# Kernel tuning notes

Measured on AMD Instinct MI355X. Metric: run time of the kernel, lower is better.

## Reference

```python
import jax, jax.numpy as jnp
import numpy as np
import math

B, L, D, K = 1, 2048, 512, 64


def setup_inputs() -> dict:
    key = jax.random.key(0)
    ks = jax.random.split(key, 12)
    w = lambda k, shape: (jax.random.normal(k, shape, jnp.float32) * 0.02)
    return {
        "x": jax.random.normal(ks[0], (B, L, D), jnp.float32),
        # key_encoder: Linear(D,D) -> GELU -> Linear(D,K)  (weights stored (in,out))
        "ke_w1": w(ks[1], (D, D)), "ke_b1": jnp.zeros((D,), jnp.float32),
        "ke_w2": w(ks[2], (D, K)), "ke_b2": jnp.zeros((K,), jnp.float32),
        # query_encoder
        "qe_w1": w(ks[3], (D, D)), "qe_b1": jnp.zeros((D,), jnp.float32),
        "qe_w2": w(ks[4], (D, K)), "qe_b2": jnp.zeros((K,), jnp.float32),
        # to_amp: Linear(D,K) -> Softplus
        "amp_w": w(ks[5], (D, K)), "amp_b": jnp.zeros((K,), jnp.float32),
        # to_value: Linear(D,D)
        "v_w": w(ks[6], (D, D)), "v_b": jnp.zeros((D,), jnp.float32),
        # to_out: LayerNorm(D) -> Linear(D,D)
        "ln_g": jnp.ones((D,), jnp.float32), "ln_b": jnp.zeros((D,), jnp.float32),
        "out_w": w(ks[7], (D, D)), "out_b": jnp.zeros((D,), jnp.float32),
    }


def reference(x, ke_w1, ke_b1, ke_w2, ke_b2, qe_w1, qe_b1, qe_w2, qe_b2,
              amp_w, amp_b, v_w, v_b, ln_g, ln_b, out_w, out_b):
    Bx, Lx, Dx = x.shape
    Kx = amp_w.shape[1]
    gelu = lambda t: jax.nn.gelu(t, approximate=False)  # torch nn.GELU default (exact)

    key_phase = jnp.tanh(gelu(x @ ke_w1 + ke_b1) @ ke_w2 + ke_b2) * math.pi   # (B,L,K)
    query_phase = jnp.tanh(gelu(x @ qe_w1 + qe_b1) @ qe_w2 + qe_b2) * math.pi  # (B,L,K)
    amp = jax.nn.softplus(x @ amp_w + amp_b) + 0.1                             # (B,L,K)
    V = x @ v_w + v_b                                                           # (B,L,D), real

    # complex phasors expressed in real arithmetic (V is real):
    # key_phasor   = amp * exp(i*key_phase)   = kr + i*ki
    # query_phasor = amp * exp(i*query_phase) = qr + i*qi
    kr = amp * jnp.cos(key_phase); ki = amp * jnp.sin(key_phase)
    qr = amp * jnp.cos(query_phase); qi = amp * jnp.sin(query_phase)

    # bound = key_phasor[...,None] * V[...,None,:]; memory = cumsum over L
    mem_r = jnp.cumsum(kr[..., None] * V[..., None, :], axis=1)  # (B,L,K,D)
    mem_i = jnp.cumsum(ki[..., None] * V[..., None, :], axis=1)  # (B,L,K,D)

    # retrieved = Re(memory * conj(query_phasor)).sum(K) = sum_k mem_r*qr + mem_i*qi
    retrieved = (jnp.einsum('blkd,blk->bld', mem_r, qr)
                 + jnp.einsum('blkd,blk->bld', mem_i, qi))        # (B,L,D)

    positions = jnp.arange(1, Lx + 1, dtype=jnp.float32)
    norm = jnp.sqrt(positions * Kx)[None, :, None]
    retrieved = retrieved / norm

    # to_out: LayerNorm(eps=1e-5) then Linear
    mu = retrieved.mean(-1, keepdims=True)
    var = ((retrieved - mu) ** 2).mean(-1, keepdims=True)
    rn = (retrieved - mu) / jnp.sqrt(var + 1e-5) * ln_g + ln_b
    return x + rn @ out_w + out_b
```

## Files before the change

kernel.cpp:

```cpp
#include <hip/hip_runtime.h>
#include <math.h>

#define L_ 2048
#define D_ 512
#define K_ 64

typedef __attribute__((ext_vector_type(8))) short short8;
typedef __attribute__((ext_vector_type(4))) float f32x4;
typedef __attribute__((ext_vector_type(4))) unsigned short us4;

__device__ __forceinline__ unsigned short f2bf(float f) {
    unsigned int u = __builtin_bit_cast(unsigned int, f);
    u += 0x7fffu + ((u >> 16) & 1u);
    return (unsigned short)(u >> 16);
}
__device__ __forceinline__ float bf2f(unsigned int u) {
    return __builtin_bit_cast(float, u << 16);
}
__device__ __forceinline__ f32x4 MFMA(short8 a, short8 b, f32x4 c) {
    return __builtin_amdgcn_mfma_f32_16x16x32_bf16(a, b, c, 0, 0, 0);
}

enum { EPI_BIAS = 0, EPI_GELU = 1, EPI_AMP = 2, EPI_PHASE = 3, EPI_OUT = 4 };

template<int EPI>
__device__ __forceinline__ void gemm_body(
    const unsigned short* __restrict__ A, const unsigned short* __restrict__ Bt,
    const float* __restrict__ bias, int N, int Kd, int m0, int n0,
    unsigned short* __restrict__ Cb, float* __restrict__ Cf,
    const float* __restrict__ extra,
    unsigned short* As, unsigned short* Bs)
{
    const int t = threadIdx.x;
    const int w = t >> 6, lane = t & 63, n_ = lane & 15, quad = lane >> 4;
    const int mh = (w >> 1) * 32, nh = (w & 1) * 32;

    f32x4 acc[2][2];
#pragma unroll
    for (int i = 0; i < 2; i++)
#pragma unroll
        for (int j = 0; j < 2; j++) acc[i][j] = (f32x4){0.f, 0.f, 0.f, 0.f};

    const int sr = t >> 2, sseg = (t & 3) * 16;
    const unsigned short* Ap = &A[(size_t)(m0 + sr) * Kd + sseg];
    const unsigned short* Bp = &Bt[(size_t)(n0 + sr) * Kd + sseg];
    const int swoff = sr * 72 + sseg;

    short8 av0 = *(const short8*)(Ap);
    short8 av1 = *(const short8*)(Ap + 8);
    short8 bv0 = *(const short8*)(Bp);
    short8 bv1 = *(const short8*)(Bp + 8);

    int buf = 0;
    *(short8*)(As + swoff) = av0; *(short8*)(As + swoff + 8) = av1;
    *(short8*)(Bs + swoff) = bv0; *(short8*)(Bs + swoff + 8) = bv1;
    __syncthreads();

    for (int k0 = 0; k0 < Kd; k0 += 64) {
        const bool more = (k0 + 64 < Kd);
        if (more) {
            av0 = *(const short8*)(Ap + k0 + 64);
            av1 = *(const short8*)(Ap + k0 + 72);
            bv0 = *(const short8*)(Bp + k0 + 64);
            bv1 = *(const short8*)(Bp + k0 + 72);
        }
        const unsigned short* Ab = As + buf * 4608;
        const unsigned short* Bb = Bs + buf * 4608;
#pragma unroll
        for (int kc = 0; kc < 2; kc++) {
            short8 a0 = *(const short8*)&Ab[(mh      + n_) * 72 + kc * 32 + quad * 8];
            short8 a1 = *(const short8*)&Ab[(mh + 16 + n_) * 72 + kc * 32 + quad * 8];
            short8 b0 = *(const short8*)&Bb[(nh      + n_) * 72 + kc * 32 + quad * 8];
            short8 b1 = *(const short8*)&Bb[(nh + 16 + n_) * 72 + kc * 32 + quad * 8];
            acc[0][0] = MFMA(a0, b0, acc[0][0]);
            acc[0][1] = MFMA(a0, b1, acc[0][1]);
            acc[1][0] = MFMA(a1, b0, acc[1][0]);
            acc[1][1] = MFMA(a1, b1, acc[1][1]);
        }
        if (more) {
            buf ^= 1;
            unsigned short* Aw = As + buf * 4608 + swoff;
            unsigned short* Bw = Bs + buf * 4608 + swoff;
            *(short8*)Aw = av0; *(short8*)(Aw + 8) = av1;
            *(short8*)Bw = bv0; *(short8*)(Bw + 8) = bv1;
            __syncthreads();
        }
    }

#pragma unroll
    for (int i = 0; i < 2; i++) {
#pragma unroll
        for (int j = 0; j < 2; j++) {
            const int mb = m0 + mh + i * 16 + quad * 4;
            const int nb = n0 + nh + j * 16 + n_;
            const float bsv = bias[nb];
#pragma unroll
            for (int reg = 0; reg < 4; reg++) {
                const int m = mb + reg;
                float v = acc[i][j][reg] + bsv;
                if (EPI == EPI_GELU) {
                    v = 0.5f * v * (1.0f + erff(v * 0.70710678118654752f));
                    Cb[(size_t)m * N + nb] = f2bf(v);
                } else if (EPI == EPI_BIAS) {
                    Cb[(size_t)m * N + nb] = f2bf(v);
                } else if (EPI == EPI_AMP) {
                    float u = (v > 20.f) ? v : log1pf(expf(v));
                    Cf[(size_t)m * N + nb] = u + 0.1f;
                } else if (EPI == EPI_PHASE) {
                    float am = extra[(size_t)m * 64 + nb];
                    float p = tanhf(v) * 3.14159265358979323846f;
                    float sp, cp; sincosf(p, &sp, &cp);
                    Cb[(size_t)m * 128 + nb]      = f2bf(am * cp);
                    Cb[(size_t)m * 128 + 64 + nb] = f2bf(am * sp);
                } else {
                    Cf[(size_t)m * N + nb] = v + extra[(size_t)m * N + nb];
                }
            }
        }
    }
}

__global__ __launch_bounds__(256)
void prep_k(const float* x, unsigned short* xb,
            const float* s0, const float* s1, const float* s2, const float* s3,
            const float* s4, const float* s5, const float* s6,
            unsigned short* d0, unsigned short* d1, unsigned short* d2, unsigned short* d3,
            unsigned short* d4, unsigned short* d5, unsigned short* d6)
{
    const int t = threadIdx.x;
    if (blockIdx.z == 7) {
        const int b = blockIdx.y * 16 + blockIdx.x;
        const float4* src = (const float4*)x;
#pragma unroll
        for (int j = 0; j < 4; j++) {
            const int idx = b * 1024 + j * 256 + t;
            float4 v = src[idx];
            us4 o;
            o.x = f2bf(v.x); o.y = f2bf(v.y); o.z = f2bf(v.z); o.w = f2bf(v.w);
            *(us4*)&xb[(size_t)idx * 4] = o;
        }
        return;
    }
    const float* S; unsigned short* D; int C;
    switch (blockIdx.z) {
        case 0: S = s0; D = d0; C = 512; break;
        case 1: S = s1; D = d1; C = 512; break;
        case 2: S = s2; D = d2; C = 512; break;
        case 3: S = s3; D = d3; C = 512; break;
        case 4: S = s4; D = d4; C = 64;  break;
        case 5: S = s5; D = d5; C = 64;  break;
        default: S = s6; D = d6; C = 64; break;
    }
    const int R = 512;
    int c0 = blockIdx.x * 32, r0 = blockIdx.y * 32;
    if (c0 >= C) return;
    __shared__ float tile[32][33];
    int r = t >> 3, c4 = (t & 7) * 4;
    float4 v = *(const float4*)&S[(size_t)(r0 + r) * C + c0 + c4];
    tile[r][c4 + 0] = v.x; tile[r][c4 + 1] = v.y;
    tile[r][c4 + 2] = v.z; tile[r][c4 + 3] = v.w;
    __syncthreads();
    us4 o;
    o.x = f2bf(tile[c4 + 0][r]); o.y = f2bf(tile[c4 + 1][r]);
    o.z = f2bf(tile[c4 + 2][r]); o.w = f2bf(tile[c4 + 3][r]);
    *(us4*)&D[(size_t)(c0 + r) * R + r0 + c4] = o;
}

__global__ __launch_bounds__(256)
void qkva_k(const unsigned short* __restrict__ xb,
            const unsigned short* wtke1, const unsigned short* wtqe1,
            const unsigned short* wtv, const unsigned short* wtamp,
            const float* ke_b1, const float* qe_b1, const float* v_b, const float* amp_b,
            unsigned short* hk, unsigned short* hq, unsigned short* Vb, float* amp)
{
    __shared__ unsigned short As[2 * 4608];
    __shared__ unsigned short Bs[2 * 4608];
    const int b = blockIdx.x;
    if (b < 768) {
        const int which = b >> 8, wi = b & 255;
        const int m0 = (wi >> 3) * 64, n0 = (wi & 7) * 64;
        if (which == 0)
            gemm_body<EPI_GELU>(xb, wtke1, ke_b1, 512, 512, m0, n0, hk, nullptr, nullptr, As, Bs);
        else if (which == 1)
            gemm_body<EPI_GELU>(xb, wtqe1, qe_b1, 512, 512, m0, n0, hq, nullptr, nullptr, As, Bs);
        else
            gemm_body<EPI_BIAS>(xb, wtv, v_b, 512, 512, m0, n0, Vb, nullptr, nullptr, As, Bs);
    } else {
        const int m0 = (b - 768) * 64;
        gemm_body<EPI_AMP>(xb, wtamp, amp_b, 64, 512, m0, 0, nullptr, amp, nullptr, As, Bs);
    }
}

__global__ __launch_bounds__(256)
void phtv_k(const unsigned short* __restrict__ hk, const unsigned short* __restrict__ hq,
            const unsigned short* wtke2, const unsigned short* wtqe2,
            const float* ke_b2, const float* qe_b2, const float* ampv,
            unsigned short* Kp, unsigned short* Qp,
            const unsigned short* __restrict__ Vb, unsigned short* __restrict__ Vt)
{
    __shared__ unsigned short As[2 * 4608];
    __shared__ unsigned short Bs[2 * 4608];
    const int b = blockIdx.x;
    if (b < 64) {
        const int m0 = (b & 31) * 64;
        if (b < 32)
            gemm_body<EPI_PHASE>(hk, wtke2, ke_b2, 64, 512, m0, 0, Kp, nullptr, ampv, As, Bs);
        else
            gemm_body<EPI_PHASE>(hq, wtqe2, qe_b2, 64, 512, m0, 0, Qp, nullptr, ampv, As, Bs);
    } else {
        const int bb = b - 64;
        const int c0 = (bb & 15) * 32, r0 = (bb >> 4) * 32;
        unsigned short (*tile)[33] = (unsigned short (*)[33])As;
        const int t = threadIdx.x, r = t >> 3, c4 = (t & 7) * 4;
        us4 v = *(const us4*)&Vb[(size_t)(r0 + r) * 512 + c0 + c4];
        tile[r][c4 + 0] = v.x; tile[r][c4 + 1] = v.y;
        tile[r][c4 + 2] = v.z; tile[r][c4 + 3] = v.w;
        __syncthreads();
        us4 o;
        o.x = tile[c4 + 0][r]; o.y = tile[c4 + 1][r];
        o.z = tile[c4 + 2][r]; o.w = tile[c4 + 3][r];
        *(us4*)&Vt[(size_t)(c0 + r) * 2048 + r0 + c4] = o;
    }
}

__global__ __launch_bounds__(256)
void attm_k(const unsigned short* __restrict__ Qp, const unsigned short* __restrict__ Kp,
            const unsigned short* __restrict__ Vt, unsigned short* __restrict__ P, int ng)
{
    __shared__ unsigned short Ss[32 * 56];

    const int t = threadIdx.x;
    const int g = blockIdx.x, lt = blockIdx.y;
    const int l0 = lt * 32;
    const int w = t >> 6, lane = t & 63, n_ = lane & 15, quad = lane >> 4;
    const int lh = (w >> 1) * 16, th = (w & 1) * 16;

    short8 qf[4];
    {
        const unsigned short* qrow = &Qp[(size_t)(l0 + lh + n_) * 128 + quad * 8];
#pragma unroll
        for (int kc = 0; kc < 4; kc++) qf[kc] = *(const short8*)(qrow + kc * 32);
    }

    f32x4 acc[2][8];
#pragma unroll
    for (int i = 0; i < 2; i++)
#pragma unroll
        for (int j = 0; j < 8; j++) acc[i][j] = (f32x4){0.f, 0.f, 0.f, 0.f};

    for (int tile = g; tile <= lt; tile += ng) {
        const int t0 = tile * 32;
        const unsigned short* krow = &Kp[(size_t)(t0 + th + n_) * 128 + quad * 8];
        f32x4 s = (f32x4){0.f, 0.f, 0.f, 0.f};
#pragma unroll
        for (int kc = 0; kc < 4; kc++)
            s = MFMA(qf[kc], *(const short8*)(krow + kc * 32), s);

        const int lrow = lh + quad * 4;
        if (tile == lt) {
            const int tg = t0 + th + n_;
#pragma unroll
            for (int reg = 0; reg < 4; reg++) {
                float v = (tg <= l0 + lrow + reg) ? s[reg] : 0.f;
                Ss[(lrow + reg) * 56 + th + n_] = f2bf(v);
            }
        } else {
#pragma unroll
            for (int reg = 0; reg < 4; reg++)
                Ss[(lrow + reg) * 56 + th + n_] = f2bf(s[reg]);
        }
        __syncthreads();

        short8 sa0 = *(const short8*)&Ss[n_ * 56 + quad * 8];
        short8 sa1 = *(const short8*)&Ss[(16 + n_) * 56 + quad * 8];
        const unsigned short* vrow = &Vt[(size_t)(w * 128 + n_) * 2048 + t0 + quad * 8];
#pragma unroll
        for (int jc = 0; jc < 8; jc++) {
            short8 vf = *(const short8*)(vrow + (size_t)jc * 16 * 2048);
            acc[0][jc] = MFMA(sa0, vf, acc[0][jc]);
            acc[1][jc] = MFMA(sa1, vf, acc[1][jc]);
        }
        __syncthreads();
    }

    unsigned short* Pg = &P[((size_t)g * L_ + l0) * 512];
#pragma unroll
    for (int i = 0; i < 2; i++) {
#pragma unroll
        for (int jc = 0; jc < 8; jc++) {
            const int row = i * 16 + quad * 4;
            const int d = w * 128 + jc * 16 + n_;
#pragma unroll
            for (int reg = 0; reg < 4; reg++)
                Pg[(size_t)(row + reg) * 512 + d] = f2bf(acc[i][jc][reg]);
        }
    }
}

__global__ __launch_bounds__(256)
void redln_k(const unsigned short* __restrict__ P, int ng,
             const float* __restrict__ lng, const float* __restrict__ lnb,
             unsigned short* __restrict__ rnb)
{
    const int l = blockIdx.x, t = threadIdx.x;
    float rx = 0.f, ry = 0.f;
    for (int gi = 0; gi < ng; gi++) {
        unsigned int p = *(const unsigned int*)&P[((size_t)gi * L_ + l) * 512 + 2 * t];
        rx += bf2f(p & 0xffffu);
        ry += bf2f(p >> 16);
    }
    const float scale = rsqrtf((float)((l + 1) * K_));
    rx *= scale; ry *= scale;

    float s = rx + ry, s2 = rx * rx + ry * ry;
    __shared__ float sb[8];
#pragma unroll
    for (int o = 32; o > 0; o >>= 1) {
        s  += __shfl_down(s,  o);
        s2 += __shfl_down(s2, o);
    }
    if ((t & 63) == 0) { int wv = t >> 6; sb[wv] = s; sb[4 + wv] = s2; }
    __syncthreads();
    s  = sb[0] + sb[1] + sb[2] + sb[3];
    s2 = sb[4] + sb[5] + sb[6] + sb[7];

    const float mu   = s * (1.f / 512.f);
    const float var  = s2 * (1.f / 512.f) - mu * mu;
    const float rstd = rsqrtf(var + 1e-5f);

    const int d = t << 1;
    rnb[(size_t)l * 512 + d]     = f2bf((rx - mu) * rstd * lng[d]     + lnb[d]);
    rnb[(size_t)l * 512 + d + 1] = f2bf((ry - mu) * rstd * lng[d + 1] + lnb[d + 1]);
}

__global__ __launch_bounds__(256)
void outg_k(const unsigned short* __restrict__ rnb, const unsigned short* wtout,
            const float* out_b, const float* __restrict__ x, float* __restrict__ out)
{
    __shared__ unsigned short As[2 * 4608];
    __shared__ unsigned short Bs[2 * 4608];
    const int wi = blockIdx.x;
    const int m0 = (wi >> 3) * 64, n0 = (wi & 7) * 64;
    gemm_body<EPI_OUT>(rnb, wtout, out_b, 512, 512, m0, n0, nullptr, out, x, As, Bs);
}

extern "C" void kernel_launch(void* const* d_in, const int* in_sizes, int n_in,
                              void* d_out, int out_size, void* d_ws, size_t ws_size,
                              hipStream_t stream)
{
    const float* x     = (const float*)d_in[0];
    const float* ke_w1 = (const float*)d_in[1];
    const float* ke_b1 = (const float*)d_in[2];
    const float* ke_w2 = (const float*)d_in[3];
    const float* ke_b2 = (const float*)d_in[4];
    const float* qe_w1 = (const float*)d_in[5];
    const float* qe_b1 = (const float*)d_in[6];
    const float* qe_w2 = (const float*)d_in[7];
    const float* qe_b2 = (const float*)d_in[8];
    const float* amp_w = (const float*)d_in[9];
    const float* amp_b = (const float*)d_in[10];
    const float* v_w   = (const float*)d_in[11];
    const float* v_b   = (const float*)d_in[12];
    const float* ln_g  = (const float*)d_in[13];
    const float* ln_b  = (const float*)d_in[14];
    const float* out_w = (const float*)d_in[15];
    const float* out_b = (const float*)d_in[16];
    float* out = (float*)d_out;
    char*  wsb = (char*)d_ws;

    unsigned short* xb    = (unsigned short*)(wsb + 0);
    unsigned short* hk    = (unsigned short*)(wsb + 2097152);
    unsigned short* hq    = (unsigned short*)(wsb + 4194304);
    unsigned short* Vb    = (unsigned short*)(wsb + 6291456);
    unsigned short* Vt    = (unsigned short*)(wsb + 8388608);
    unsigned short* Qp    = (unsigned short*)(wsb + 10485760);
    unsigned short* Kp    = (unsigned short*)(wsb + 11010048);
    float*          amp   = (float*)(wsb + 11534336);
    unsigned short* rnb   = (unsigned short*)(wsb + 12058624);
    unsigned short* wtke1 = (unsigned short*)(wsb + 14155776);
    unsigned short* wtqe1 = (unsigned short*)(wsb + 14680064);
    unsigned short* wtv   = (unsigned short*)(wsb + 15204352);
    unsigned short* wtout = (unsigned short*)(wsb + 15728640);
    unsigned short* wtke2 = (unsigned short*)(wsb + 16252928);
    unsigned short* wtqe2 = (unsigned short*)(wsb + 16318464);
    unsigned short* wtamp = (unsigned short*)(wsb + 16384000);
    unsigned short* P     = (unsigned short*)(wsb + 16449536);

    const size_t base_bytes = 16449536ull;
    const size_t per_group  = 2097152ull;
    int ng = 1;
    if (ws_size > base_bytes + per_group) {
        size_t n = (ws_size - base_bytes) / per_group;
        ng = (n > 8) ? 8 : (int)n;
        if (ng < 1) ng = 1;
    }

    dim3 blk(256);
    prep_k<<<dim3(16, 16, 8), blk, 0, stream>>>(x, xb,
                                                ke_w1, qe_w1, v_w, out_w, ke_w2, qe_w2, amp_w,
                                                wtke1, wtqe1, wtv, wtout, wtke2, wtqe2, wtamp);
    qkva_k<<<dim3(800), blk, 0, stream>>>(xb, wtke1, wtqe1, wtv, wtamp,
                                          ke_b1, qe_b1, v_b, amp_b, hk, hq, Vb, amp);
    phtv_k<<<dim3(1088), blk, 0, stream>>>(hk, hq, wtke2, wtqe2, ke_b2, qe_b2, amp,
                                           Kp, Qp, Vb, Vt);
    attm_k<<<dim3(ng, 64), blk, 0, stream>>>(Qp, Kp, Vt, P, ng);
    redln_k<<<dim3(L_), blk, 0, stream>>>(P, ng, ln_g, ln_b, rnb);
    outg_k<<<dim3(256), blk, 0, stream>>>(rnb, wtout, out_b, x, out);
}
```

Measured before the change: 155.3 us.

## Fuse reduce+LayerNorm into attention, batch tiles, split phase GEMM finer

Removes the separate reduction/LayerNorm kernel. The last attention block for each row tile, detected with an atomic counter, sums the partial results across groups and applies LayerNorm in place. The attention loop now computes GRP score tiles before one barrier and then does the V updates, which cuts the number of syncs per tile. The phase GEMM gets a dedicated 32-row kernel that launches twice as many blocks, and the GEMM tile order is swapped to column-major. The cost is an atomic/threadfence tail where one block does the serial LN work for its row tile.

Measured after the change: 270.6 us. +74.2%, slower.

```diff
diff --git a/kernel.cpp b/kernel.cpp
--- a/kernel.cpp
+++ b/kernel.cpp
@@ -4,10 +4,12 @@
 #define L_ 2048
 #define D_ 512
 #define K_ 64
+#define GRP 4
 
 typedef __attribute__((ext_vector_type(8))) short short8;
 typedef __attribute__((ext_vector_type(4))) float f32x4;
 typedef __attribute__((ext_vector_type(4))) unsigned short us4;
+typedef __attribute__((ext_vector_type(8))) unsigned short us8;
 
 __device__ __forceinline__ unsigned short f2bf(float f) {
     unsigned int u = __builtin_bit_cast(unsigned int, f);
@@ -21,7 +23,7 @@
     return __builtin_amdgcn_mfma_f32_16x16x32_bf16(a, b, c, 0, 0, 0);
 }
 
-enum { EPI_BIAS = 0, EPI_GELU = 1, EPI_AMP = 2, EPI_PHASE = 3, EPI_OUT = 4 };
+enum { EPI_BIAS = 0, EPI_GELU = 1, EPI_AMP = 2, EPI_OUT = 4 };
 
 template<int EPI>
 __device__ __forceinline__ void gemm_body(
@@ -106,12 +108,6 @@
                 } else if (EPI == EPI_AMP) {
                     float u = (v > 20.f) ? v : log1pf(expf(v));
                     Cf[(size_t)m * N + nb] = u + 0.1f;
-                } else if (EPI == EPI_PHASE) {
-                    float am = extra[(size_t)m * 64 + nb];
-                    float p = tanhf(v) * 3.14159265358979323846f;
-                    float sp, cp; sincosf(p, &sp, &cp);
-                    Cb[(size_t)m * 128 + nb]      = f2bf(am * cp);
-                    Cb[(size_t)m * 128 + 64 + nb] = f2bf(am * sp);
                 } else {
                     Cf[(size_t)m * N + nb] = v + extra[(size_t)m * N + nb];
                 }
@@ -120,8 +116,82 @@
     }
 }
 
+__device__ __forceinline__ void phase_body(
+    const unsigned short* __restrict__ A, const unsigned short* __restrict__ Bt,
+    const float* __restrict__ bias, int m0,
+    unsigned short* __restrict__ Cb, const float* __restrict__ amp,
+    unsigned short* As, unsigned short* Bs)
+{
+    const int t = threadIdx.x;
+    const int w = t >> 6, lane = t & 63, n_ = lane & 15, quad = lane >> 4;
+    const int Kd = 512;
+
+    f32x4 acc[2];
+    acc[0] = (f32x4){0.f, 0.f, 0.f, 0.f};
+    acc[1] = (f32x4){0.f, 0.f, 0.f, 0.f};
+
+    const int arow = t >> 3, aseg = (t & 7) * 8;
+    const int brow = t >> 2, bseg = (t & 3) * 16;
+    const unsigned short* Ap = &A[(size_t)(m0 + arow) * Kd + aseg];
+    const unsigned short* Bp = &Bt[(size_t)brow * Kd + bseg];
+    const int aoff = arow * 72 + aseg;
+    const int boff = brow * 72 + bseg;
+
+    short8 av  = *(const short8*)Ap;
+    short8 bv0 = *(const short8*)Bp;
+    short8 bv1 = *(const short8*)(Bp + 8);
+
+    int buf = 0;
+    *(short8*)(As + aoff) = av;
+    *(short8*)(Bs + boff) = bv0; *(short8*)(Bs + boff + 8) = bv1;
+    __syncthreads();
+
+    for (int k0 = 0; k0 < Kd; k0 += 64) {
+        const bool more = (k0 + 64 < Kd);
+        if (more) {
+            av  = *(const short8*)(Ap + k0 + 64);
+            bv0 = *(const short8*)(Bp + k0 + 64);
+            bv1 = *(const short8*)(Bp + k0 + 72);
+        }
+        const unsigned short* Ab = As + buf * 2304;
+        const unsigned short* Bb = Bs + buf * 4608;
+#pragma unroll
+        for (int kc = 0; kc < 2; kc++) {
+            short8 a0 = *(const short8*)&Ab[(n_)      * 72 + kc * 32 + quad * 8];
+            short8 a1 = *(const short8*)&Ab[(16 + n_) * 72 + kc * 32 + quad * 8];
+            short8 b0 = *(const short8*)&Bb[(w * 16 + n_) * 72 + kc * 32 + quad * 8];
+            acc[0] = MFMA(a0, b0, acc[0]);
+            acc[1] = MFMA(a1, b0, acc[1]);
+        }
+        if (more) {
+            buf ^= 1;
+            *(short8*)(As + buf * 2304 + aoff) = av;
+            *(short8*)(Bs + buf * 4608 + boff) = bv0;
+            *(short8*)(Bs + buf * 4608 + boff + 8) = bv1;
+            __syncthreads();
+        }
+    }
+
+    const int nb = w * 16 + n_;
+    const float bsv = bias[nb];
+#pragma unroll
+    for (int i = 0; i < 2; i++) {
+        const int mb = m0 + i * 16 + quad * 4;
+#pragma unroll
+        for (int reg = 0; reg < 4; reg++) {
+            const int m = mb + reg;
+            float v = acc[i][reg] + bsv;
+            float am = amp[(size_t)m * 64 + nb];
+            float p = tanhf(v) * 3.14159265358979323846f;
+            float sp, cp; sincosf(p, &sp, &cp);
+            Cb[(size_t)m * 128 + nb]      = f2bf(am * cp);
+            Cb[(size_t)m * 128 + 64 + nb] = f2bf(am * sp);
+        }
+    }
+}
+
 __global__ __launch_bounds__(256)
-void prep_k(const float* x, unsigned short* xb,
+void prep_k(const float* x, unsigned short* xb, int* cnt,
             const float* s0, const float* s1, const float* s2, const float* s3,
             const float* s4, const float* s5, const float* s6,
             unsigned short* d0, unsigned short* d1, unsigned short* d2, unsigned short* d3,
@@ -129,6 +199,7 @@
 {
     const int t = threadIdx.x;
     if (blockIdx.z == 7) {
+        if (blockIdx.x == 0 && blockIdx.y == 0 && t < 64) cnt[t] = 0;
         const int b = blockIdx.y * 16 + blockIdx.x;
         const float4* src = (const float4*)x;
 #pragma unroll
@@ -178,7 +249,7 @@
     const int b = blockIdx.x;
     if (b < 768) {
         const int which = b >> 8, wi = b & 255;
-        const int m0 = (wi >> 3) * 64, n0 = (wi & 7) * 64;
+        const int m0 = (wi & 31) * 64, n0 = (wi >> 5) * 64;
         if (which == 0)
             gemm_body<EPI_GELU>(xb, wtke1, ke_b1, 512, 512, m0, n0, hk, nullptr, nullptr, As, Bs);
         else if (which == 1)
@@ -198,17 +269,16 @@
             unsigned short* Kp, unsigned short* Qp,
             const unsigned short* __restrict__ Vb, unsigned short* __restrict__ Vt)
 {
-    __shared__ unsigned short As[2 * 4608];
+    __shared__ unsigned short As[2 * 2304];
     __shared__ unsigned short Bs[2 * 4608];
     const int b = blockIdx.x;
-    if (b < 64) {
-        const int m0 = (b & 31) * 64;
-        if (b < 32)
-            gemm_body<EPI_PHASE>(hk, wtke2, ke_b2, 64, 512, m0, 0, Kp, nullptr, ampv, As, Bs);
+    if (b < 128) {
+        if (b < 64)
+            phase_body(hk, wtke2, ke_b2, b * 32, Kp, ampv, As, Bs);
         else
-            gemm_body<EPI_PHASE>(hq, wtqe2, qe_b2, 64, 512, m0, 0, Qp, nullptr, ampv, As, Bs);
+            phase_body(hq, wtqe2, qe_b2, (b - 64) * 32, Qp, ampv, As, Bs);
     } else {
-        const int bb = b - 64;
+        const int bb = b - 128;
         const int c0 = (bb & 15) * 32, r0 = (bb >> 4) * 32;
         unsigned short (*tile)[33] = (unsigned short (*)[33])As;
         const int t = threadIdx.x, r = t >> 3, c4 = (t & 7) * 4;
@@ -225,9 +295,12 @@
 
 __global__ __launch_bounds__(256)
 void attm_k(const unsigned short* __restrict__ Qp, const unsigned short* __restrict__ Kp,
-            const unsigned short* __restrict__ Vt, unsigned short* __restrict__ P, int ng)
-{
-    __shared__ unsigned short Ss[32 * 56];
+            const unsigned short* __restrict__ Vt, unsigned short* __restrict__ P, int ng,
+            int* __restrict__ cnt, const float* __restrict__ lng, const float* __restrict__ lnb,
+            unsigned short* __restrict__ rnb)
+{
+    __shared__ unsigned short Ss[GRP][32 * 56];
+    __shared__ int sdone;
 
     const int t = threadIdx.x;
     const int g = blockIdx.x, lt = blockIdx.y;
@@ -248,37 +321,46 @@
 #pragma unroll
         for (int j = 0; j < 8; j++) acc[i][j] = (f32x4){0.f, 0.f, 0.f, 0.f};
 
-    for (int tile = g; tile <= lt; tile += ng) {
-        const int t0 = tile * 32;
-        const unsigned short* krow = &Kp[(size_t)(t0 + th + n_) * 128 + quad * 8];
-        f32x4 s = (f32x4){0.f, 0.f, 0.f, 0.f};
-#pragma unroll
-        for (int kc = 0; kc < 4; kc++)
-            s = MFMA(qf[kc], *(const short8*)(krow + kc * 32), s);
-
-        const int lrow = lh + quad * 4;
-        if (tile == lt) {
-            const int tg = t0 + th + n_;
-#pragma unroll
-            for (int reg = 0; reg < 4; reg++) {
-                float v = (tg <= l0 + lrow + reg) ? s[reg] : 0.f;
-                Ss[(lrow + reg) * 56 + th + n_] = f2bf(v);
-            }
-        } else {
-#pragma unroll
-            for (int reg = 0; reg < 4; reg++)
-                Ss[(lrow + reg) * 56 + th + n_] = f2bf(s[reg]);
+    for (int ta = g; ta <= lt; ta += GRP * ng) {
+#pragma unroll
+        for (int p = 0; p < GRP; p++) {
+            const int tile = ta + p * ng;
+            if (tile > lt) continue;
+            const int t0 = tile * 32;
+            const unsigned short* krow = &Kp[(size_t)(t0 + th + n_) * 128 + quad * 8];
+            f32x4 s = (f32x4){0.f, 0.f, 0.f, 0.f};
+#pragma unroll
+            for (int kc = 0; kc < 4; kc++)
+                s = MFMA(qf[kc], *(const short8*)(krow + kc * 32), s);
+            const int lrow = lh + quad * 4;
+            if (tile == lt) {
+                const int tg = t0 + th + n_;
+#pragma unroll
+                for (int reg = 0; reg < 4; reg++) {
+                    float v = (tg <= l0 + lrow + reg) ? s[reg] : 0.f;
+                    Ss[p][(lrow + reg) * 56 + th + n_] = f2bf(v);
+                }
+            } else {
+#pragma unroll
+                for (int reg = 0; reg < 4; reg++)
+                    Ss[p][(lrow + reg) * 56 + th + n_] = f2bf(s[reg]);
+            }
         }
         __syncthreads();
-
-        short8 sa0 = *(const short8*)&Ss[n_ * 56 + quad * 8];
-        short8 sa1 = *(const short8*)&Ss[(16 + n_) * 56 + quad * 8];
-        const unsigned short* vrow = &Vt[(size_t)(w * 128 + n_) * 2048 + t0 + quad * 8];
-#pragma unroll
-        for (int jc = 0; jc < 8; jc++) {
-            short8 vf = *(const short8*)(vrow + (size_t)jc * 16 * 2048);
-            acc[0][jc] = MFMA(sa0, vf, acc[0][jc]);
-            acc[1][jc] = MFMA(sa1, vf, acc[1][jc]);
+#pragma unroll
+        for (int p = 0; p < GRP; p++) {
+            const int tile = ta + p * ng;
+            if (tile > lt) continue;
+            const int t0 = tile * 32;
+            short8 sa0 = *(const short8*)&Ss[p][n_ * 56 + quad * 8];
+            short8 sa1 = *(const short8*)&Ss[p][(16 + n_) * 56 + quad * 8];
+            const unsigned short* vrow = &Vt[(size_t)(w * 128 + n_) * 2048 + t0 + quad * 8];
+#pragma unroll
+            for (int jc = 0; jc < 8; jc++) {
+                short8 vf = *(const short8*)(vrow + (size_t)jc * 16 * 2048);
+                acc[0][jc] = MFMA(sa0, vf, acc[0][jc]);
+                acc[1][jc] = MFMA(sa1, vf, acc[1][jc]);
+            }
         }
         __syncthreads();
     }
@@ -295,42 +377,44 @@
                 Pg[(size_t)(row + reg) * 512 + d] = f2bf(acc[i][jc][reg]);
         }
     }
-}
-
-__global__ __launch_bounds__(256)
-void redln_k(const unsigned short* __restrict__ P, int ng,
-             const float* __restrict__ lng, const float* __restrict__ lnb,
-             unsigned short* __restrict__ rnb)
-{
-    const int l = blockIdx.x, t = threadIdx.x;
-    float rx = 0.f, ry = 0.f;
-    for (int gi = 0; gi < ng; gi++) {
-        unsigned int p = *(const unsigned int*)&P[((size_t)gi * L_ + l) * 512 + 2 * t];
-        rx += bf2f(p & 0xffffu);
-        ry += bf2f(p >> 16);
-    }
-    const float scale = rsqrtf((float)((l + 1) * K_));
-    rx *= scale; ry *= scale;
-
-    float s = rx + ry, s2 = rx * rx + ry * ry;
-    __shared__ float sb[8];
-#pragma unroll
-    for (int o = 32; o > 0; o >>= 1) {
-        s  += __shfl_down(s,  o);
-        s2 += __shfl_down(s2, o);
-    }
-    if ((t & 63) == 0) { int wv = t >> 6; sb[wv] = s; sb[4 + wv] = s2; }
+
+    __threadfence();
+    if (t == 0) sdone = atomicAdd(&cnt[lt], 1);
     __syncthreads();
-    s  = sb[0] + sb[1] + sb[2] + sb[3];
-    s2 = sb[4] + sb[5] + sb[6] + sb[7];
-
-    const float mu   = s * (1.f / 512.f);
-    const float var  = s2 * (1.f / 512.f) - mu * mu;
-    const float rstd = rsqrtf(var + 1e-5f);
-
-    const int d = t << 1;
-    rnb[(size_t)l * 512 + d]     = f2bf((rx - mu) * rstd * lng[d]     + lnb[d]);
-    rnb[(size_t)l * 512 + d + 1] = f2bf((ry - mu) * rstd * lng[d + 1] + lnb[d + 1]);
+    if (sdone == ng - 1) {
+        __threadfence();
+        for (int rr = w; rr < 32; rr += 4) {
+            const int l = l0 + rr;
+            float v[8];
+#pragma unroll
+            for (int j = 0; j < 8; j++) v[j] = 0.f;
+            for (int gi = 0; gi < ng; gi++) {
+                us8 pk = *(const us8*)&P[((size_t)gi * L_ + l) * 512 + lane * 8];
+#pragma unroll
+                for (int j = 0; j < 8; j++) v[j] += bf2f((unsigned int)pk[j]);
+            }
+            const float scale = rsqrtf((float)((l + 1) * K_));
+            float s = 0.f, s2 = 0.f;
+#pragma unroll
+            for (int j = 0; j < 8; j++) {
+                v[j] *= scale;
+                s += v[j]; s2 += v[j] * v[j];
+            }
+#pragma unroll
+            for (int o = 32; o > 0; o >>= 1) {
+                s  += __shfl_xor(s,  o);
+                s2 += __shfl_xor(s2, o);
+            }
+            const float mu   = s * (1.f / 512.f);
+            const float var  = s2 * (1.f / 512.f) - mu * mu;
+            const float rstd = rsqrtf(var + 1e-5f);
+#pragma unroll
+            for (int j = 0; j < 8; j++) {
+                const int d = lane * 8 + j;
+                rnb[(size_t)l * 512 + d] = f2bf((v[j] - mu) * rstd * lng[d] + lnb[d]);
+            }
+        }
+    }
 }
 
 __global__ __launch_bounds__(256)
@@ -340,7 +424,7 @@
     __shared__ unsigned short As[2 * 4608];
     __shared__ unsigned short Bs[2 * 4608];
     const int wi = blockIdx.x;
-    const int m0 = (wi >> 3) * 64, n0 = (wi & 7) * 64;
+    const int m0 = (wi & 31) * 64, n0 = (wi >> 5) * 64;
     gemm_body<EPI_OUT>(rnb, wtout, out_b, 512, 512, m0, n0, nullptr, out, x, As, Bs);
 }
 
@@ -384,9 +468,10 @@
     unsigned short* wtke2 = (unsigned short*)(wsb + 16252928);
     unsigned short* wtqe2 = (unsigned short*)(wsb + 16318464);
     unsigned short* wtamp = (unsigned short*)(wsb + 16384000);
-    unsigned short* P     = (unsigned short*)(wsb + 16449536);
-
-    const size_t base_bytes = 16449536ull;
+    int*            cnt   = (int*)(wsb + 16449536);
+    unsigned short* P     = (unsigned short*)(wsb + 16449792);
+
+    const size_t base_bytes = 16449792ull;
     const size_t per_group  = 2097152ull;
     int ng = 1;
     if (ws_size > base_bytes + per_group) {
@@ -396,14 +481,13 @@
     }
 
     dim3 blk(256);
-    prep_k<<<dim3(16, 16, 8), blk, 0, stream>>>(x, xb,
+    prep_k<<<dim3(16, 16, 8), blk, 0, stream>>>(x, xb, cnt,
                                                 ke_w1, qe_w1, v_w, out_w, ke_w2, qe_w2, amp_w,
                                                 wtke1, wtqe1, wtv, wtout, wtke2, wtqe2, wtamp);
     qkva_k<<<dim3(800), blk, 0, stream>>>(xb, wtke1, wtqe1, wtv, wtamp,
                                           ke_b1, qe_b1, v_b, amp_b, hk, hq, Vb, amp);
-    phtv_k<<<dim3(1088), blk, 0, stream>>>(hk, hq, wtke2, wtqe2, ke_b2, qe_b2, amp,
+    phtv_k<<<dim3(1152), blk, 0, stream>>>(hk, hq, wtke2, wtqe2, ke_b2, qe_b2, amp,
                                            Kp, Qp, Vb, Vt);
-    attm_k<<<dim3(ng, 64), blk, 0, stream>>>(Qp, Kp, Vt, P, ng);
-    redln_k<<<dim3(L_), blk, 0, stream>>>(P, ng, ln_g, ln_b, rnb);
+    attm_k<<<dim3(ng, 64), blk, 0, stream>>>(Qp, Kp, Vt, P, ng, cnt, ln_g, ln_b, rnb);
     outg_k<<<dim3(256), blk, 0, stream>>>(rnb, wtout, out_b, x, out);
 }
```
